# Kernel tuning notes

Hardware: AMD Instinct MI355X
Metric: run time of the kernel (lower is better)

Reference implementation:

```python
import jax, jax.numpy as jnp
import numpy as np

B, T, D, H, OUT = 4096, 48, 59, 256, 1


def _uni(k, shape, fan_in):
    s = 1.0 / np.sqrt(fan_in)
    return jax.random.uniform(k, shape, jnp.float32, -s, s)


def setup_inputs() -> dict:
    key = jax.random.key(0)
    ks = jax.random.split(key, 16)
    return {
        "x": jax.random.normal(ks[0], (B, T, D), jnp.float32),
        "mask": (jax.random.uniform(ks[1], (B, T, D)) < 0.7).astype(jnp.float32),
        "deltas": jax.random.uniform(ks[2], (B, T, D), jnp.float32) * 5.0,
        "last_obs": jax.random.normal(ks[3], (B, D), jnp.float32),
        "h": jax.random.normal(ks[4], (B, H), jnp.float32) * 0.1,
        "medians": jnp.zeros((D,), jnp.float32),  # medians_df=None -> zeros
        # Decay temp_decay_h (non-diag)
        "W_dh": _uni(ks[5], (H, D), D), "b_dh": jnp.zeros((H,), jnp.float32),
        # Decay temp_decay_x (diag, input==output)
        "W_dx": _uni(ks[6], (D, D), D), "b_dx": jnp.zeros((D,), jnp.float32),
        # hist: Linear(H, D)
        "hist_W": _uni(ks[7], (D, H), H), "hist_b": jnp.zeros((D,), jnp.float32),
        "feat_W": _uni(ks[8], (D, D), D), "feat_b": jnp.zeros((D,), jnp.float32),
        # weight_combine: Linear(2D, D)
        "wcomb_W": _uni(ks[9], (D, 2 * D), 2 * D), "wcomb_b": jnp.zeros((D,), jnp.float32),
        # Decay_obs linear (D, D)
        "wobs_W": _uni(ks[10], (D, D), D), "wobs_b": jnp.zeros((D,), jnp.float32),
        # GRUCell(2D, H)
        "W_ih": _uni(ks[11], (3 * H, 2 * D), 2 * D),
        "W_hh": _uni(ks[12], (3 * H, H), H),
        "b_ih": jnp.zeros((3 * H,), jnp.float32),
        "b_hh": jnp.zeros((3 * H,), jnp.float32),
        # classification: Linear(H, OUT)
        "cls_W": _uni(ks[13], (OUT, H), H), "cls_b": jnp.zeros((OUT,), jnp.float32),
    }


def reference(x, mask, deltas, last_obs, h, medians,
              W_dh, b_dh, W_dx, b_dx, hist_W, hist_b, feat_W, feat_b,
              wcomb_W, wcomb_b, wobs_W, wobs_b,
              W_ih, W_hh, b_ih, b_hh, cls_W, cls_b):
    Dn = x.shape[-1]
    Hn = h.shape[-1]
    eye = jnp.eye(Dn, dtype=x.dtype)

    # Decay_obs: sign-gated tanh weighting of (deltas - medians)
    dd = deltas - medians[None, None, :]
    wd = jnp.einsum('btd,ed->bte', dd, wobs_W) + wobs_b
    # relu(wd) + relu(-wd) == |wd|
    decay_factor = 0.5 * (1.0 - jnp.tanh(jnp.sign(dd) * jnp.abs(wd)))  # [B,T,D]

    dx_diag = jnp.diagonal(W_dx)          # diag decay: W * eye
    feat_Wm = feat_W * (1.0 - eye)

    def step(h, ins):
        x_t, m_t, d_t = ins               # each [B,D]
        gamma_h = jnp.exp(-jax.nn.relu(d_t @ W_dh.T + b_dh))   # [B,H]
        h = h * gamma_h
        x_h = h @ hist_W.T + hist_b                              # history estimate [B,D]
        x_r = m_t * x_t + (1.0 - m_t) * x_h                      # complemented input
        xu = x_r @ feat_Wm.T + feat_b
        gamma_x = jnp.exp(-jax.nn.relu(d_t * dx_diag + b_dx))    # diag decay [B,D]
        beta = jax.nn.sigmoid(
            jnp.concatenate([gamma_x, m_t], axis=-1) @ wcomb_W.T + wcomb_b)
        x_comb = beta * xu + (1.0 - beta) * x_h
        loss_t = jnp.sum(jnp.abs(x_t - x_comb) * m_t) / (jnp.sum(m_t) + 1e-5)
        x_imp_t = m_t * x_t + (1.0 - m_t) * x_comb
        # GRUCell with input concat([x_imp_t, m_t])
        gi = jnp.concatenate([x_imp_t, m_t], axis=-1) @ W_ih.T + b_ih
        gh = h @ W_hh.T + b_hh
        r = jax.nn.sigmoid(gi[:, :Hn] + gh[:, :Hn])
        z = jax.nn.sigmoid(gi[:, Hn:2 * Hn] + gh[:, Hn:2 * Hn])
        n = jnp.tanh(gi[:, 2 * Hn:] + r * gh[:, 2 * Hn:])
        h_new = (1.0 - z) * n + z * h
        return h_new, (x_imp_t, h_new, loss_t)

    xs = (x.transpose(1, 0, 2), mask.transpose(1, 0, 2), deltas.transpose(1, 0, 2))
    h_last, (x_imp, hs, losses) = jax.lax.scan(step, h, xs)
    x_imp = x_imp.transpose(1, 0, 2)          # [B,T,D]
    hidden_states = hs.transpose(1, 0, 2)     # [B,T,H]
    x_loss = jnp.sum(losses)
    y_out = h_last @ cls_W.T + cls_b          # dropout = identity at eval
    y_score = jax.nn.sigmoid(y_out)
    return x_imp, x_loss, hidden_states, y_out, y_score, decay_factor
```

## Files before the change

kernel.cpp:

```cpp
#include <hip/hip_runtime.h>
#include <math.h>

#define BATCH 4096
#define TT 48
#define DDIM 59
#define HHID 256
#define RR 16
#define NWG (BATCH/RR)
#define NTHR 1024

typedef _Float16 f16;
typedef _Float16 f16x8 __attribute__((ext_vector_type(8)));
typedef float    f32x4 __attribute__((ext_vector_type(4)));

static constexpr size_t N_XIMP   = (size_t)BATCH*TT*DDIM;
static constexpr size_t OFF_LOSS = N_XIMP;
static constexpr size_t OFF_HS   = OFF_LOSS + 1;
static constexpr size_t N_HS     = (size_t)BATCH*TT*HHID;
static constexpr size_t OFF_YOUT = OFF_HS + N_HS;
static constexpr size_t OFF_YSC  = OFF_YOUT + BATCH;
static constexpr size_t OFF_DEC  = OFF_YSC + BATCH;

static constexpr size_t WOFF_GRU  = 0;
static constexpr size_t WOFF_DH   = 294912;
static constexpr size_t WOFF_HIST = 311296;
static constexpr size_t WOFF_FEAT = 327680;
static constexpr size_t WOFF_WC   = 331776;

__device__ __forceinline__ float sigm(float v){ return 1.f/(1.f+expf(-v)); }

__global__ __launch_bounds__(256) void decay_kernel(
    const float* __restrict__ deltas, const float* __restrict__ medians,
    const float* __restrict__ wobs_W, const float* __restrict__ wobs_b,
    float* __restrict__ out_decay)
{
  __shared__ float sW[DDIM][60];
  __shared__ float sb[64], smed[64];
  __shared__ float sdd[16][60];
  const int tid = threadIdx.x;
  for (int idx = tid; idx < DDIM*DDIM; idx += 256){
    int e = idx/DDIM, d = idx - e*DDIM;
    sW[e][d] = wobs_W[idx];
  }
  if (tid < DDIM){ sb[tid] = wobs_b[tid]; smed[tid] = medians[tid]; }
  __syncthreads();
  const size_t row0 = (size_t)blockIdx.x * 16;
  for (int idx = tid; idx < 16*DDIM; idx += 256){
    int r = idx/DDIM, d = idx - r*DDIM;
    sdd[r][d] = __builtin_nontemporal_load(&deltas[(row0+r)*DDIM + d]) - smed[d];
  }
  __syncthreads();
  for (int idx = tid; idx < 16*DDIM; idx += 256){
    int r = idx/DDIM, e = idx - r*DDIM;
    float acc = sb[e];
    for (int d = 0; d < DDIM; d++) acc += sdd[r][d]*sW[e][d];
    float dd = sdd[r][e];
    float sg = (dd > 0.f) ? 1.f : ((dd < 0.f) ? -1.f : 0.f);
    out_decay[(row0+r)*DDIM + e] = 0.5f*(1.f - tanhf(sg*fabsf(acc)));
  }
}

__global__ __launch_bounds__(256) void conv_kernel(
    const float* __restrict__ W_dh, const float* __restrict__ hist_W,
    const float* __restrict__ feat_W, const float* __restrict__ wcomb_W,
    const float* __restrict__ W_ih, const float* __restrict__ W_hh,
    f16* __restrict__ ws)
{
  const int g  = blockIdx.x*4 + (threadIdx.x >> 6);
  const int l  = threadIdx.x & 63;
  const int nl = l & 15;
  const int kh = (l >> 4) * 8;
  f16x8 out;
  if (g < 576){
    int jb = g/36, s = g - jb*36;
    if (s < 24){
      int gate = s/12, kt = s - gate*12;
      int row  = gate*256 + jb*16 + nl;
      #pragma unroll
      for (int e = 0; e < 8; e++){
        int k = kt*32 + kh + e;
        float v = (k < 256) ? W_hh[(size_t)row*256 + k]
                : (k < 374) ? W_ih[(size_t)row*118 + (k-256)] : 0.f;
        out[e] = (f16)v;
      }
    } else if (s < 32){
      int kt = s - 24, row = 512 + jb*16 + nl;
      #pragma unroll
      for (int e = 0; e < 8; e++){
        int k = kt*32 + kh + e;
        out[e] = (f16)W_hh[(size_t)row*256 + k];
      }
    } else {
      int kt = s - 32, row = 512 + jb*16 + nl;
      #pragma unroll
      for (int e = 0; e < 8; e++){
        int k = kt*32 + kh + e;
        out[e] = (f16)((k < 118) ? W_ih[(size_t)row*118 + k] : 0.f);
      }
    }
    *(f16x8*)&ws[WOFF_GRU + (size_t)g*512 + l*8] = out;
  } else if (g < 608){
    int i = g - 576, nt = i >> 1, kt = i & 1;
    int row = nt*16 + nl;
    #pragma unroll
    for (int e = 0; e < 8; e++){
      int k = kt*32 + kh + e;
      out[e] = (f16)((k < 59) ? W_dh[(size_t)row*59 + k] : 0.f);
    }
    *(f16x8*)&ws[WOFF_DH + (size_t)i*512 + l*8] = out;
  } else if (g < 640){
    int i = g - 608, nt = i >> 3, kt = i & 7;
    int n = nt*16 + nl;
    #pragma unroll
    for (int e = 0; e < 8; e++){
      int k = kt*32 + kh + e;
      out[e] = (f16)((n < 59) ? hist_W[(size_t)n*256 + k] : 0.f);
    }
    *(f16x8*)&ws[WOFF_HIST + (size_t)i*512 + l*8] = out;
  } else if (g < 648){
    int i = g - 640, nt = i >> 1, kt = i & 1;
    int n = nt*16 + nl;
    #pragma unroll
    for (int e = 0; e < 8; e++){
      int k = kt*32 + kh + e;
      out[e] = (f16)((n < 59 && k < 59 && k != n) ? feat_W[(size_t)n*59 + k] : 0.f);
    }
    *(f16x8*)&ws[WOFF_FEAT + (size_t)i*512 + l*8] = out;
  } else {
    int i = g - 648, nt = i >> 2, kt = i & 3;
    int n = nt*16 + nl;
    #pragma unroll
    for (int e = 0; e < 8; e++){
      int k = kt*32 + kh + e;
      out[e] = (f16)((n < 59 && k < 118) ? wcomb_W[(size_t)n*118 + k] : 0.f);
    }
    *(f16x8*)&ws[WOFF_WC + (size_t)i*512 + l*8] = out;
  }
}

__global__ __launch_bounds__(NTHR) void seq_kernel(
    const float* __restrict__ x, const float* __restrict__ mask,
    const float* __restrict__ deltas, const float* __restrict__ h0,
    const float* __restrict__ b_dh, const float* __restrict__ W_dx,
    const float* __restrict__ b_dx, const float* __restrict__ hist_b,
    const float* __restrict__ feat_b, const float* __restrict__ wcomb_b,
    const float* __restrict__ b_ih, const float* __restrict__ b_hh,
    const f16* __restrict__ wb,
    float* __restrict__ out_ximp, float* __restrict__ out_hs,
    float* __restrict__ ws_num, float* __restrict__ ws_den)
{
  __shared__ f16 Acat[RR*392];
  __shared__ f16 AdAxr[RR*72];
  __shared__ f16 Agm [RR*136];
  __shared__ f16 ssx [RR*60];
  __shared__ f16 sxh [RR*60];
  __shared__ f16 sxu [RR*60];
  __shared__ f16 sbt [RR*60];
  __shared__ float sh [RR*260];
  __shared__ float sdiag[64], sbdx[64];
  __shared__ float sredN[16], sredD[16];

  const int tid = threadIdx.x;
  const int w   = tid >> 6;
  const int l   = tid & 63;
  const int nl  = l & 15;
  const int kh  = (l >> 4) * 8;
  const int mq  = (l >> 4) * 4;
  const int row0 = blockIdx.x * RR;

  const f16* Bgru  = wb + WOFF_GRU;
  const f16* Bdh   = wb + WOFF_DH;
  const f16* Bhist = wb + WOFF_HIST;
  const f16* Bfeat = wb + WOFF_FEAT;
  const f16* Bwc   = wb + WOFF_WC;
  const f16* Bb    = Bgru + (size_t)w*36*512;

  const bool hasS = (tid < RR*DDIM);
  const int r0s = tid/59, d0s = tid - r0s*59;

  const int nG = w*16 + nl;
  const float bdh_n = b_dh[nG];
  const float br_j  = b_ih[nG]     + b_hh[nG];
  const float bz_j  = b_ih[256+nG] + b_hh[256+nG];
  const float bni_j = b_ih[512+nG];
  const float bnh_j = b_hh[512+nG];
  const int nA = w*16 + nl;
  const int nB = (w-4)*16 + nl;
  const float hb_n = (w < 4 && nA < DDIM) ? hist_b[nA] : 0.f;
  const float fb_n = (w < 4 && nA < DDIM) ? feat_b[nA] : 0.f;
  const float cb_n = (w >= 4 && w < 8 && nB < DDIM) ? wcomb_b[nB] : 0.f;

  if (tid < DDIM){ sdiag[tid] = W_dx[(size_t)tid*DDIM + tid]; sbdx[tid] = b_dx[tid]; }
  for (int idx = tid; idx < RR*18; idx += NTHR){
    int r = idx/18, c = idx - (idx/18)*18;
    Acat[r*392 + 374 + c] = (f16)0.f;
    Agm [r*136 + 118 + c] = (f16)0.f;
  }
  for (int idx = tid; idx < RR*13; idx += NTHR){
    int r = idx/13, c = idx - (idx/13)*13;
    AdAxr[r*72 + 59 + c] = (f16)0.f;
  }
  for (int idx = tid; idx < RR*HHID; idx += NTHR){
    int r = idx >> 8, j = idx & 255;
    sh[r*260 + j] = h0[(size_t)(row0+r)*HHID + j];
  }

  float vx0 = 0.f, vm0 = 0.f, vd0 = 0.f;
  if (hasS){
    size_t g0 = ((size_t)(row0+r0s)*TT)*DDIM + d0s;
    vx0 = __builtin_nontemporal_load(&x[g0]);
    vm0 = __builtin_nontemporal_load(&mask[g0]);
    vd0 = __builtin_nontemporal_load(&deltas[g0]);
  }
  __syncthreads();

  for (int t = 0; t < TT; t++){
    if (hasS){
      ssx[r0s*60+d0s] = (f16)vx0;
      AdAxr[r0s*72+d0s] = (f16)vd0;
      Agm[r0s*136+59+d0s] = (f16)vm0;
      Acat[r0s*392+315+d0s] = (f16)vm0;
    }
    __syncthreads();

    if (t + 1 < TT && hasS){
      size_t g0 = ((size_t)(row0+r0s)*TT + (t+1))*DDIM + d0s;
      vx0 = __builtin_nontemporal_load(&x[g0]);
      vm0 = __builtin_nontemporal_load(&mask[g0]);
      vd0 = __builtin_nontemporal_load(&deltas[g0]);
    }

    {
      f32x4 acc = {0.f,0.f,0.f,0.f};
      #pragma unroll
      for (int kt = 0; kt < 2; kt++){
        f16x8 a = *(const f16x8*)&AdAxr[nl*72 + kt*32 + kh];
        f16x8 b = *(const f16x8*)&Bdh[(size_t)(w*2+kt)*512 + l*8];
        acc = __builtin_amdgcn_mfma_f32_16x16x32_f16(a, b, acc, 0, 0, 0);
      }
      #pragma unroll
      for (int q = 0; q < 4; q++){
        float gm = expf(-fmaxf(acc[q] + bdh_n, 0.f));
        float hv = sh[(mq+q)*260 + nG] * gm;
        sh[(mq+q)*260 + nG] = hv;
        Acat[(mq+q)*392 + nG] = (f16)hv;
      }
      if (hasS){
        float dv = (float)AdAxr[r0s*72 + d0s];
        float gx = expf(-fmaxf(dv*sdiag[d0s] + sbdx[d0s], 0.f));
        Agm[r0s*136 + d0s] = (f16)gx;
      }
    }
    __syncthreads();

    f32x4 gr = {0.f,0.f,0.f,0.f}, gz = {0.f,0.f,0.f,0.f}, gnh = {0.f,0.f,0.f,0.f};
    {
      #pragma unroll
      for (int kt = 0; kt < 8; kt++){
        f16x8 a  = *(const f16x8*)&Acat[nl*392 + kt*32 + kh];
        f16x8 br = *(const f16x8*)&Bb[(size_t)kt*512 + l*8];
        f16x8 bz = *(const f16x8*)&Bb[(size_t)(12+kt)*512 + l*8];
        f16x8 bn = *(const f16x8*)&Bb[(size_t)(24+kt)*512 + l*8];
        gr  = __builtin_amdgcn_mfma_f32_16x16x32_f16(a, br, gr, 0, 0, 0);
        gz  = __builtin_amdgcn_mfma_f32_16x16x32_f16(a, bz, gz, 0, 0, 0);
        gnh = __builtin_amdgcn_mfma_f32_16x16x32_f16(a, bn, gnh, 0, 0, 0);
      }
      if (w < 4){
        f32x4 acc = {0.f,0.f,0.f,0.f};
        #pragma unroll
        for (int kt = 0; kt < 8; kt++){
          f16x8 a = *(const f16x8*)&Acat[nl*392 + kt*32 + kh];
          f16x8 b = *(const f16x8*)&Bhist[(size_t)(w*8+kt)*512 + l*8];
          acc = __builtin_amdgcn_mfma_f32_16x16x32_f16(a, b, acc, 0, 0, 0);
        }
        if (nA < DDIM){
          #pragma unroll
          for (int q = 0; q < 4; q++) sxh[(mq+q)*60 + nA] = (f16)(acc[q] + hb_n);
        }
      } else if (w < 8){
        f32x4 acc = {0.f,0.f,0.f,0.f};
        #pragma unroll
        for (int kt = 0; kt < 4; kt++){
          f16x8 a = *(const f16x8*)&Agm[nl*136 + kt*32 + kh];
          f16x8 b = *(const f16x8*)&Bwc[(size_t)((w-4)*4+kt)*512 + l*8];
          acc = __builtin_amdgcn_mfma_f32_16x16x32_f16(a, b, acc, 0, 0, 0);
        }
        if (nB < DDIM){
          #pragma unroll
          for (int q = 0; q < 4; q++) sbt[(mq+q)*60 + nB] = (f16)sigm(acc[q] + cb_n);
        }
      }
    }
    __syncthreads();

    if (hasS){
      float m  = (float)Acat[r0s*392 + 315 + d0s];
      float xr = m*(float)ssx[r0s*60+d0s] + (1.f-m)*(float)sxh[r0s*60+d0s];
      AdAxr[r0s*72+d0s] = (f16)xr;
    }
    __syncthreads();

    if (w < 4){
      f32x4 acc = {0.f,0.f,0.f,0.f};
      #pragma unroll
      for (int kt = 0; kt < 2; kt++){
        f16x8 a = *(const f16x8*)&AdAxr[nl*72 + kt*32 + kh];
        f16x8 b = *(const f16x8*)&Bfeat[(size_t)(w*2+kt)*512 + l*8];
        acc = __builtin_amdgcn_mfma_f32_16x16x32_f16(a, b, acc, 0, 0, 0);
      }
      if (nA < DDIM){
        #pragma unroll
        for (int q = 0; q < 4; q++) sxu[(mq+q)*60 + nA] = (f16)(acc[q] + fb_n);
      }
    }
    __syncthreads();

    float lnum = 0.f, lden = 0.f;
    if (hasS){
      float xh = (float)sxh[r0s*60+d0s], xu = (float)sxu[r0s*60+d0s];
      float bt = (float)sbt[r0s*60+d0s];
      float xc = bt*xu + (1.f-bt)*xh;
      float m  = (float)Acat[r0s*392 + 315 + d0s];
      float xv = (float)ssx[r0s*60+d0s];
      lnum = fabsf(xv - xc)*m;
      lden = m;
      float xi = m*xv + (1.f-m)*xc;
      Acat[r0s*392 + 256 + d0s] = (f16)xi;
      out_ximp[((size_t)(row0+r0s)*TT + t)*DDIM + d0s] = xi;
    }
    #pragma unroll
    for (int off = 32; off >= 1; off >>= 1){
      lnum += __shfl_xor(lnum, off);
      lden += __shfl_xor(lden, off);
    }
    if (l == 0){ sredN[w] = lnum; sredD[w] = lden; }
    __syncthreads();
    if (tid == 0){
      float a = 0.f, b = 0.f;
      #pragma unroll
      for (int k = 0; k < 16; k++){ a += sredN[k]; b += sredD[k]; }
      atomicAdd(&ws_num[t], a); atomicAdd(&ws_den[t], b);
    }

    {
      f32x4 gni = {0.f,0.f,0.f,0.f};
      #pragma unroll
      for (int kt = 8; kt < 12; kt++){
        f16x8 a  = *(const f16x8*)&Acat[nl*392 + kt*32 + kh];
        f16x8 br = *(const f16x8*)&Bb[(size_t)kt*512 + l*8];
        f16x8 bz = *(const f16x8*)&Bb[(size_t)(12+kt)*512 + l*8];
        f16x8 bn = *(const f16x8*)&Bb[(size_t)(32+kt-8)*512 + l*8];
        gr  = __builtin_amdgcn_mfma_f32_16x16x32_f16(a, br, gr, 0, 0, 0);
        gz  = __builtin_amdgcn_mfma_f32_16x16x32_f16(a, bz, gz, 0, 0, 0);
        gni = __builtin_amdgcn_mfma_f32_16x16x32_f16(a, bn, gni, 0, 0, 0);
      }
      #pragma unroll
      for (int q = 0; q < 4; q++){
        float rg = sigm(gr[q] + br_j);
        float zg = sigm(gz[q] + bz_j);
        float ng = tanhf(gni[q] + bni_j + rg*(gnh[q] + bnh_j));
        float hold = sh[(mq+q)*260 + nG];
        float hn = (1.f-zg)*ng + zg*hold;
        sh[(mq+q)*260 + nG] = hn;
        __builtin_nontemporal_store(hn, &out_hs[((size_t)(row0+mq+q)*TT + t)*HHID + nG]);
      }
    }
    __syncthreads();
  }
}

__global__ __launch_bounds__(256) void final_kernel(
    const float* __restrict__ hs, const float* __restrict__ cls_W,
    const float* __restrict__ cls_b, const float* __restrict__ ws_num,
    const float* __restrict__ ws_den, float* __restrict__ out)
{
  int b = blockIdx.x*256 + threadIdx.x;
  if (b < BATCH){
    const float* hr = hs + ((size_t)b*TT + (TT-1))*HHID;
    float acc = cls_b[0];
    for (int j = 0; j < HHID; j++) acc += hr[j]*cls_W[j];
    out[OFF_YOUT + b] = acc;
    out[OFF_YSC  + b] = sigm(acc);
  }
  if (blockIdx.x == 0 && threadIdx.x == 0){
    float s = 0.f;
    for (int tt = 0; tt < TT; tt++) s += ws_num[tt]/(ws_den[tt] + 1e-5f);
    out[OFF_LOSS] = s;
  }
}

extern "C" void kernel_launch(void* const* d_in, const int* in_sizes, int n_in,
                              void* d_out, int out_size, void* d_ws, size_t ws_size,
                              hipStream_t stream)
{
  const float* x       = (const float*)d_in[0];
  const float* mask_   = (const float*)d_in[1];
  const float* deltas  = (const float*)d_in[2];
  const float* h0      = (const float*)d_in[4];
  const float* medians = (const float*)d_in[5];
  const float* W_dh    = (const float*)d_in[6];
  const float* b_dh    = (const float*)d_in[7];
  const float* W_dx    = (const float*)d_in[8];
  const float* b_dx    = (const float*)d_in[9];
  const float* hist_W  = (const float*)d_in[10];
  const float* hist_b  = (const float*)d_in[11];
  const float* feat_W  = (const float*)d_in[12];
  const float* feat_b  = (const float*)d_in[13];
  const float* wcomb_W = (const float*)d_in[14];
  const float* wcomb_b = (const float*)d_in[15];
  const float* wobs_W  = (const float*)d_in[16];
  const float* wobs_b  = (const float*)d_in[17];
  const float* W_ih    = (const float*)d_in[18];
  const float* W_hh    = (const float*)d_in[19];
  const float* b_ih    = (const float*)d_in[20];
  const float* b_hh    = (const float*)d_in[21];
  const float* cls_W   = (const float*)d_in[22];
  const float* cls_b   = (const float*)d_in[23];

  float* out    = (float*)d_out;
  float* ws_num = (float*)d_ws;
  float* ws_den = ws_num + TT;
  f16*   wbase  = (f16*)((char*)d_ws + 512);

  hipMemsetAsync(d_ws, 0, 512, stream);

  conv_kernel<<<166, 256, 0, stream>>>(W_dh, hist_W, feat_W, wcomb_W,
                                       W_ih, W_hh, wbase);

  decay_kernel<<<BATCH*TT/16, 256, 0, stream>>>(deltas, medians, wobs_W, wobs_b,
                                                out + OFF_DEC);

  seq_kernel<<<NWG, NTHR, 0, stream>>>(x, mask_, deltas, h0,
      b_dh, W_dx, b_dx, hist_b, feat_b, wcomb_b, b_ih, b_hh, wbase,
      out , out + OFF_HS, ws_num, ws_den);

  final_kernel<<<BATCH/256, 256, 0, stream>>>(out + OFF_HS, cls_W, cls_b,
                                              ws_num, ws_den, out);
}
```

Measured before the change: 1.524 ms.

## Halve seq_kernel block to 512 threads with two output tiles per wave

```diff
diff --git a/kernel.cpp b/kernel.cpp
--- a/kernel.cpp
+++ b/kernel.cpp
@@ -7,7 +7,7 @@
 #define HHID 256
 #define RR 16
 #define NWG (BATCH/RR)
-#define NTHR 1024
+#define NTHR 512
 
 typedef _Float16 f16;
 typedef _Float16 f16x8 __attribute__((ext_vector_type(8)));
@@ -138,7 +138,7 @@
   }
 }
 
-__global__ __launch_bounds__(NTHR) void seq_kernel(
+__global__ __launch_bounds__(NTHR, 2) void seq_kernel(
     const float* __restrict__ x, const float* __restrict__ mask,
     const float* __restrict__ deltas, const float* __restrict__ h0,
     const float* __restrict__ b_dh, const float* __restrict__ W_dx,
@@ -150,15 +150,14 @@
     float* __restrict__ ws_num, float* __restrict__ ws_den)
 {
   __shared__ f16 Acat[RR*392];
-  __shared__ f16 AdAxr[RR*72];
+  __shared__ f16 Ad  [RR*72];
   __shared__ f16 Agm [RR*136];
   __shared__ f16 ssx [RR*60];
   __shared__ f16 sxh [RR*60];
   __shared__ f16 sxu [RR*60];
   __shared__ f16 sbt [RR*60];
   __shared__ float sh [RR*260];
-  __shared__ float sdiag[64], sbdx[64];
-  __shared__ float sredN[16], sredD[16];
+  __shared__ float sredN[8], sredD[8];
 
   const int tid = threadIdx.x;
   const int w   = tid >> 6;
@@ -173,24 +172,38 @@
   const f16* Bhist = wb + WOFF_HIST;
   const f16* Bfeat = wb + WOFF_FEAT;
   const f16* Bwc   = wb + WOFF_WC;
-  const f16* Bb    = Bgru + (size_t)w*36*512;
-
-  const bool hasS = (tid < RR*DDIM);
-  const int r0s = tid/59, d0s = tid - r0s*59;
-
-  const int nG = w*16 + nl;
-  const float bdh_n = b_dh[nG];
-  const float br_j  = b_ih[nG]     + b_hh[nG];
-  const float bz_j  = b_ih[256+nG] + b_hh[256+nG];
-  const float bni_j = b_ih[512+nG];
-  const float bnh_j = b_hh[512+nG];
+
+  const int r0s = tid/59,        d0s = tid - r0s*59;
+  const int i1  = tid + NTHR;
+  const int r1s = i1/59,         d1s = i1 - r1s*59;
+  const bool has1 = (i1 < RR*DDIM);
+
+  const float dg0 = W_dx[(size_t)d0s*DDIM + d0s], bx0 = b_dx[d0s];
+  const float dg1 = has1 ? W_dx[(size_t)d1s*DDIM + d1s] : 0.f;
+  const float bx1 = has1 ? b_dx[d1s] : 0.f;
+
+  float bdh_i[2], br_j[2], bz_j[2], bni_j[2], bnh_j[2];
+  #pragma unroll
+  for (int ii = 0; ii < 2; ii++){
+    int n = (2*w+ii)*16 + nl;
+    bdh_i[ii] = b_dh[n];
+    br_j[ii]  = b_ih[n]     + b_hh[n];
+    bz_j[ii]  = b_ih[256+n] + b_hh[256+n];
+    bni_j[ii] = b_ih[512+n];
+    bnh_j[ii] = b_hh[512+n];
+  }
   const int nA = w*16 + nl;
   const int nB = (w-4)*16 + nl;
   const float hb_n = (w < 4 && nA < DDIM) ? hist_b[nA] : 0.f;
   const float fb_n = (w < 4 && nA < DDIM) ? feat_b[nA] : 0.f;
-  const float cb_n = (w >= 4 && w < 8 && nB < DDIM) ? wcomb_b[nB] : 0.f;
-
-  if (tid < DDIM){ sdiag[tid] = W_dx[(size_t)tid*DDIM + tid]; sbdx[tid] = b_dx[tid]; }
+  const float cb_n = (w >= 4 && nB < DDIM) ? wcomb_b[nB] : 0.f;
+
+  const int hrowA = tid >> 6;
+  const int hrowB = hrowA + 8;
+  const int hj0   = (tid & 63) * 4;
+  float* hsA = out_hs + (size_t)(row0+hrowA)*TT*HHID + hj0;
+  float* hsB = out_hs + (size_t)(row0+hrowB)*TT*HHID + hj0;
+
   for (int idx = tid; idx < RR*18; idx += NTHR){
     int r = idx/18, c = idx - (idx/18)*18;
     Acat[r*392 + 374 + c] = (f16)0.f;
@@ -198,93 +211,139 @@
   }
   for (int idx = tid; idx < RR*13; idx += NTHR){
     int r = idx/13, c = idx - (idx/13)*13;
-    AdAxr[r*72 + 59 + c] = (f16)0.f;
+    Ad[r*72 + 59 + c] = (f16)0.f;
   }
   for (int idx = tid; idx < RR*HHID; idx += NTHR){
     int r = idx >> 8, j = idx & 255;
     sh[r*260 + j] = h0[(size_t)(row0+r)*HHID + j];
   }
 
-  float vx0 = 0.f, vm0 = 0.f, vd0 = 0.f;
-  if (hasS){
+  float vx0, vm0, vd0, vx1 = 0.f, vm1 = 0.f, vd1 = 0.f;
+  {
     size_t g0 = ((size_t)(row0+r0s)*TT)*DDIM + d0s;
     vx0 = __builtin_nontemporal_load(&x[g0]);
     vm0 = __builtin_nontemporal_load(&mask[g0]);
     vd0 = __builtin_nontemporal_load(&deltas[g0]);
+    if (has1){
+      size_t g1 = ((size_t)(row0+r1s)*TT)*DDIM + d1s;
+      vx1 = __builtin_nontemporal_load(&x[g1]);
+      vm1 = __builtin_nontemporal_load(&mask[g1]);
+      vd1 = __builtin_nontemporal_load(&deltas[g1]);
+    }
   }
   __syncthreads();
 
   for (int t = 0; t < TT; t++){
-    if (hasS){
-      ssx[r0s*60+d0s] = (f16)vx0;
-      AdAxr[r0s*72+d0s] = (f16)vd0;
+    {
+      ssx[r0s*60+d0s]     = (f16)vx0;
+      Ad [r0s*72+d0s]     = (f16)vd0;
       Agm[r0s*136+59+d0s] = (f16)vm0;
       Acat[r0s*392+315+d0s] = (f16)vm0;
+      Agm[r0s*136+d0s]    = (f16)expf(-fmaxf(vd0*dg0 + bx0, 0.f));
+      if (has1){
+        ssx[r1s*60+d1s]     = (f16)vx1;
+        Ad [r1s*72+d1s]     = (f16)vd1;
+        Agm[r1s*136+59+d1s] = (f16)vm1;
+        Acat[r1s*392+315+d1s] = (f16)vm1;
+        Agm[r1s*136+d1s]    = (f16)expf(-fmaxf(vd1*dg1 + bx1, 0.f));
+      }
+      if (t > 0){
+        f32x4 va, vb;
+        #pragma unroll
+        for (int c = 0; c < 4; c++){ va[c] = sh[hrowA*260 + hj0 + c]; vb[c] = sh[hrowB*260 + hj0 + c]; }
+        __builtin_nontemporal_store(va, (f32x4*)(hsA + (size_t)(t-1)*HHID));
+        __builtin_nontemporal_store(vb, (f32x4*)(hsB + (size_t)(t-1)*HHID));
+      }
     }
     __syncthreads();
 
-    if (t + 1 < TT && hasS){
+    if (t + 1 < TT){
       size_t g0 = ((size_t)(row0+r0s)*TT + (t+1))*DDIM + d0s;
       vx0 = __builtin_nontemporal_load(&x[g0]);
       vm0 = __builtin_nontemporal_load(&mask[g0]);
       vd0 = __builtin_nontemporal_load(&deltas[g0]);
+      if (has1){
+        size_t g1 = ((size_t)(row0+r1s)*TT + (t+1))*DDIM + d1s;
+        vx1 = __builtin_nontemporal_load(&x[g1]);
+        vm1 = __builtin_nontemporal_load(&mask[g1]);
+        vd1 = __builtin_nontemporal_load(&deltas[g1]);
+      }
     }
 
     {
-      f32x4 acc = {0.f,0.f,0.f,0.f};
-      #pragma unroll
-      for (int kt = 0; kt < 2; kt++){
-        f16x8 a = *(const f16x8*)&AdAxr[nl*72 + kt*32 + kh];
-        f16x8 b = *(const f16x8*)&Bdh[(size_t)(w*2+kt)*512 + l*8];
-        acc = __builtin_amdgcn_mfma_f32_16x16x32_f16(a, b, acc, 0, 0, 0);
-      }
-      #pragma unroll
-      for (int q = 0; q < 4; q++){
-        float gm = expf(-fmaxf(acc[q] + bdh_n, 0.f));
-        float hv = sh[(mq+q)*260 + nG] * gm;
-        sh[(mq+q)*260 + nG] = hv;
-        Acat[(mq+q)*392 + nG] = (f16)hv;
-      }
-      if (hasS){
-        float dv = (float)AdAxr[r0s*72 + d0s];
-        float gx = expf(-fmaxf(dv*sdiag[d0s] + sbdx[d0s], 0.f));
-        Agm[r0s*136 + d0s] = (f16)gx;
+      f16x8 a0 = *(const f16x8*)&Ad[nl*72 + kh];
+      f16x8 a1 = *(const f16x8*)&Ad[nl*72 + 32 + kh];
+      #pragma unroll
+      for (int ii = 0; ii < 2; ii++){
+        int nt = 2*w + ii;
+        f16x8 b0 = *(const f16x8*)&Bdh[(size_t)(nt*2+0)*512 + l*8];
+        f16x8 b1 = *(const f16x8*)&Bdh[(size_t)(nt*2+1)*512 + l*8];
+        f32x4 acc = {0.f,0.f,0.f,0.f};
+        acc = __builtin_amdgcn_mfma_f32_16x16x32_f16(a0, b0, acc, 0, 0, 0);
+        acc = __builtin_amdgcn_mfma_f32_16x16x32_f16(a1, b1, acc, 0, 0, 0);
+        int n = nt*16 + nl;
+        #pragma unroll
+        for (int q = 0; q < 4; q++){
+          float gm = expf(-fmaxf(acc[q] + bdh_i[ii], 0.f));
+          float hv = sh[(mq+q)*260 + n] * gm;
+          sh[(mq+q)*260 + n] = hv;
+          Acat[(mq+q)*392 + n] = (f16)hv;
+        }
       }
     }
     __syncthreads();
 
-    f32x4 gr = {0.f,0.f,0.f,0.f}, gz = {0.f,0.f,0.f,0.f}, gnh = {0.f,0.f,0.f,0.f};
+    f32x4 gr[2], gz[2], gnh[2];
     {
-      #pragma unroll
-      for (int kt = 0; kt < 8; kt++){
-        f16x8 a  = *(const f16x8*)&Acat[nl*392 + kt*32 + kh];
-        f16x8 br = *(const f16x8*)&Bb[(size_t)kt*512 + l*8];
-        f16x8 bz = *(const f16x8*)&Bb[(size_t)(12+kt)*512 + l*8];
-        f16x8 bn = *(const f16x8*)&Bb[(size_t)(24+kt)*512 + l*8];
-        gr  = __builtin_amdgcn_mfma_f32_16x16x32_f16(a, br, gr, 0, 0, 0);
-        gz  = __builtin_amdgcn_mfma_f32_16x16x32_f16(a, bz, gz, 0, 0, 0);
-        gnh = __builtin_amdgcn_mfma_f32_16x16x32_f16(a, bn, gnh, 0, 0, 0);
-      }
+      f16x8 aH[8];
+      #pragma unroll
+      for (int kt = 0; kt < 8; kt++)
+        aH[kt] = *(const f16x8*)&Acat[nl*392 + kt*32 + kh];
+
+      #pragma unroll
+      for (int jj = 0; jj < 2; jj++){
+        const f16* Bb = Bgru + (size_t)(2*w+jj)*36*512;
+        f16x8 br[8], bz[8], bn[8];
+        #pragma unroll
+        for (int kt = 0; kt < 8; kt++){
+          br[kt] = *(const f16x8*)&Bb[(size_t)kt*512 + l*8];
+          bz[kt] = *(const f16x8*)&Bb[(size_t)(12+kt)*512 + l*8];
+          bn[kt] = *(const f16x8*)&Bb[(size_t)(24+kt)*512 + l*8];
+        }
+        f32x4 r_ = {0.f,0.f,0.f,0.f}, z_ = {0.f,0.f,0.f,0.f}, n_ = {0.f,0.f,0.f,0.f};
+        #pragma unroll
+        for (int kt = 0; kt < 8; kt++){
+          r_ = __builtin_amdgcn_mfma_f32_16x16x32_f16(aH[kt], br[kt], r_, 0, 0, 0);
+          z_ = __builtin_amdgcn_mfma_f32_16x16x32_f16(aH[kt], bz[kt], z_, 0, 0, 0);
+          n_ = __builtin_amdgcn_mfma_f32_16x16x32_f16(aH[kt], bn[kt], n_, 0, 0, 0);
+        }
+        gr[jj] = r_; gz[jj] = z_; gnh[jj] = n_;
+      }
+
       if (w < 4){
+        f16x8 bh[8];
+        #pragma unroll
+        for (int kt = 0; kt < 8; kt++)
+          bh[kt] = *(const f16x8*)&Bhist[(size_t)(w*8+kt)*512 + l*8];
         f32x4 acc = {0.f,0.f,0.f,0.f};
         #pragma unroll
-        for (int kt = 0; kt < 8; kt++){
-          f16x8 a = *(const f16x8*)&Acat[nl*392 + kt*32 + kh];
-          f16x8 b = *(const f16x8*)&Bhist[(size_t)(w*8+kt)*512 + l*8];
-          acc = __builtin_amdgcn_mfma_f32_16x16x32_f16(a, b, acc, 0, 0, 0);
-        }
+        for (int kt = 0; kt < 8; kt++)
+          acc = __builtin_amdgcn_mfma_f32_16x16x32_f16(aH[kt], bh[kt], acc, 0, 0, 0);
         if (nA < DDIM){
           #pragma unroll
           for (int q = 0; q < 4; q++) sxh[(mq+q)*60 + nA] = (f16)(acc[q] + hb_n);
         }
-      } else if (w < 8){
+      } else {
+        f16x8 aG[4], bw[4];
+        #pragma unroll
+        for (int kt = 0; kt < 4; kt++){
+          aG[kt] = *(const f16x8*)&Agm[nl*136 + kt*32 + kh];
+          bw[kt] = *(const f16x8*)&Bwc[(size_t)((w-4)*4+kt)*512 + l*8];
+        }
         f32x4 acc = {0.f,0.f,0.f,0.f};
         #pragma unroll
-        for (int kt = 0; kt < 4; kt++){
-          f16x8 a = *(const f16x8*)&Agm[nl*136 + kt*32 + kh];
-          f16x8 b = *(const f16x8*)&Bwc[(size_t)((w-4)*4+kt)*512 + l*8];
-          acc = __builtin_amdgcn_mfma_f32_16x16x32_f16(a, b, acc, 0, 0, 0);
-        }
+        for (int kt = 0; kt < 4; kt++)
+          acc = __builtin_amdgcn_mfma_f32_16x16x32_f16(aG[kt], bw[kt], acc, 0, 0, 0);
         if (nB < DDIM){
           #pragma unroll
           for (int q = 0; q < 4; q++) sbt[(mq+q)*60 + nB] = (f16)sigm(acc[q] + cb_n);
@@ -293,40 +352,59 @@
     }
     __syncthreads();
 
-    if (hasS){
-      float m  = (float)Acat[r0s*392 + 315 + d0s];
-      float xr = m*(float)ssx[r0s*60+d0s] + (1.f-m)*(float)sxh[r0s*60+d0s];
-      AdAxr[r0s*72+d0s] = (f16)xr;
+    if (w < 4){
+      f16x8 bf0 = *(const f16x8*)&Bfeat[(size_t)(w*2+0)*512 + l*8];
+      f16x8 bf1 = *(const f16x8*)&Bfeat[(size_t)(w*2+1)*512 + l*8];
+      f16x8 a0, a1;
+      #pragma unroll
+      for (int e = 0; e < 8; e++){
+        int c0 = kh + e;
+        int c1 = 32 + kh + e;
+        float xr0 = 0.f, xr1 = 0.f;
+        if (c0 < DDIM){
+          float m = (float)Agm[nl*136 + 59 + c0];
+          xr0 = m*(float)ssx[nl*60 + c0] + (1.f-m)*(float)sxh[nl*60 + c0];
+        }
+        if (c1 < DDIM){
+          float m = (float)Agm[nl*136 + 59 + c1];
+          xr1 = m*(float)ssx[nl*60 + c1] + (1.f-m)*(float)sxh[nl*60 + c1];
+        }
+        a0[e] = (f16)xr0; a1[e] = (f16)xr1;
+      }
+      f32x4 acc = {0.f,0.f,0.f,0.f};
+      acc = __builtin_amdgcn_mfma_f32_16x16x32_f16(a0, bf0, acc, 0, 0, 0);
+      acc = __builtin_amdgcn_mfma_f32_16x16x32_f16(a1, bf1, acc, 0, 0, 0);
+      if (nA < DDIM){
+        #pragma unroll
+        for (int q = 0; q < 4; q++) sxu[(mq+q)*60 + nA] = (f16)(acc[q] + fb_n);
+      }
     }
     __syncthreads();
 
-    if (w < 4){
-      f32x4 acc = {0.f,0.f,0.f,0.f};
-      #pragma unroll
-      for (int kt = 0; kt < 2; kt++){
-        f16x8 a = *(const f16x8*)&AdAxr[nl*72 + kt*32 + kh];
-        f16x8 b = *(const f16x8*)&Bfeat[(size_t)(w*2+kt)*512 + l*8];
-        acc = __builtin_amdgcn_mfma_f32_16x16x32_f16(a, b, acc, 0, 0, 0);
-      }
-      if (nA < DDIM){
-        #pragma unroll
-        for (int q = 0; q < 4; q++) sxu[(mq+q)*60 + nA] = (f16)(acc[q] + fb_n);
-      }
-    }
-    __syncthreads();
-
     float lnum = 0.f, lden = 0.f;
-    if (hasS){
+    {
       float xh = (float)sxh[r0s*60+d0s], xu = (float)sxu[r0s*60+d0s];
       float bt = (float)sbt[r0s*60+d0s];
       float xc = bt*xu + (1.f-bt)*xh;
-      float m  = (float)Acat[r0s*392 + 315 + d0s];
+      float m  = (float)Agm[r0s*136 + 59 + d0s];
       float xv = (float)ssx[r0s*60+d0s];
       lnum = fabsf(xv - xc)*m;
       lden = m;
       float xi = m*xv + (1.f-m)*xc;
       Acat[r0s*392 + 256 + d0s] = (f16)xi;
       out_ximp[((size_t)(row0+r0s)*TT + t)*DDIM + d0s] = xi;
+      if (has1){
+        xh = (float)sxh[r1s*60+d1s]; xu = (float)sxu[r1s*60+d1s];
+        bt = (float)sbt[r1s*60+d1s];
+        xc = bt*xu + (1.f-bt)*xh;
+        m  = (float)Agm[r1s*136 + 59 + d1s];
+        xv = (float)ssx[r1s*60+d1s];
+        lnum += fabsf(xv - xc)*m;
+        lden += m;
+        xi = m*xv + (1.f-m)*xc;
+        Acat[r1s*392 + 256 + d1s] = (f16)xi;
+        out_ximp[((size_t)(row0+r1s)*TT + t)*DDIM + d1s] = xi;
+      }
     }
     #pragma unroll
     for (int off = 32; off >= 1; off >>= 1){
@@ -338,34 +416,54 @@
     if (tid == 0){
       float a = 0.f, b = 0.f;
       #pragma unroll
-      for (int k = 0; k < 16; k++){ a += sredN[k]; b += sredD[k]; }
+      for (int k = 0; k < 8; k++){ a += sredN[k]; b += sredD[k]; }
       atomicAdd(&ws_num[t], a); atomicAdd(&ws_den[t], b);
     }
 
     {
-      f32x4 gni = {0.f,0.f,0.f,0.f};
-      #pragma unroll
-      for (int kt = 8; kt < 12; kt++){
-        f16x8 a  = *(const f16x8*)&Acat[nl*392 + kt*32 + kh];
-        f16x8 br = *(const f16x8*)&Bb[(size_t)kt*512 + l*8];
-        f16x8 bz = *(const f16x8*)&Bb[(size_t)(12+kt)*512 + l*8];
-        f16x8 bn = *(const f16x8*)&Bb[(size_t)(32+kt-8)*512 + l*8];
-        gr  = __builtin_amdgcn_mfma_f32_16x16x32_f16(a, br, gr, 0, 0, 0);
-        gz  = __builtin_amdgcn_mfma_f32_16x16x32_f16(a, bz, gz, 0, 0, 0);
-        gni = __builtin_amdgcn_mfma_f32_16x16x32_f16(a, bn, gni, 0, 0, 0);
-      }
-      #pragma unroll
-      for (int q = 0; q < 4; q++){
-        float rg = sigm(gr[q] + br_j);
-        float zg = sigm(gz[q] + bz_j);
-        float ng = tanhf(gni[q] + bni_j + rg*(gnh[q] + bnh_j));
-        float hold = sh[(mq+q)*260 + nG];
-        float hn = (1.f-zg)*ng + zg*hold;
-        sh[(mq+q)*260 + nG] = hn;
-        __builtin_nontemporal_store(hn, &out_hs[((size_t)(row0+mq+q)*TT + t)*HHID + nG]);
+      f16x8 aT[4];
+      #pragma unroll
+      for (int k = 0; k < 4; k++)
+        aT[k] = *(const f16x8*)&Acat[nl*392 + (8+k)*32 + kh];
+      #pragma unroll
+      for (int jj = 0; jj < 2; jj++){
+        const f16* Bb = Bgru + (size_t)(2*w+jj)*36*512;
+        f16x8 br[4], bz[4], bn[4];
+        #pragma unroll
+        for (int k = 0; k < 4; k++){
+          br[k] = *(const f16x8*)&Bb[(size_t)(8+k)*512 + l*8];
+          bz[k] = *(const f16x8*)&Bb[(size_t)(20+k)*512 + l*8];
+          bn[k] = *(const f16x8*)&Bb[(size_t)(32+k)*512 + l*8];
+        }
+        f32x4 r_ = gr[jj], z_ = gz[jj];
+        f32x4 gni = {0.f,0.f,0.f,0.f};
+        #pragma unroll
+        for (int k = 0; k < 4; k++){
+          r_  = __builtin_amdgcn_mfma_f32_16x16x32_f16(aT[k], br[k], r_, 0, 0, 0);
+          z_  = __builtin_amdgcn_mfma_f32_16x16x32_f16(aT[k], bz[k], z_, 0, 0, 0);
+          gni = __builtin_amdgcn_mfma_f32_16x16x32_f16(aT[k], bn[k], gni, 0, 0, 0);
+        }
+        int j = (2*w+jj)*16 + nl;
+        #pragma unroll
+        for (int q = 0; q < 4; q++){
+          float rg = sigm(r_[q] + br_j[jj]);
+          float zg = sigm(z_[q] + bz_j[jj]);
+          float ng = tanhf(gni[q] + bni_j[jj] + rg*(gnh[jj][q] + bnh_j[jj]));
+          float hold = sh[(mq+q)*260 + j];
+          float hn = (1.f-zg)*ng + zg*hold;
+          sh[(mq+q)*260 + j] = hn;
+        }
       }
     }
     __syncthreads();
+  }
+
+  {
+    f32x4 va, vb;
+    #pragma unroll
+    for (int c = 0; c < 4; c++){ va[c] = sh[hrowA*260 + hj0 + c]; vb[c] = sh[hrowB*260 + hj0 + c]; }
+    __builtin_nontemporal_store(va, (f32x4*)(hsA + (size_t)(TT-1)*HHID));
+    __builtin_nontemporal_store(vb, (f32x4*)(hsB + (size_t)(TT-1)*HHID));
   }
 }
 
@@ -422,7 +520,7 @@
   float* ws_den = ws_num + TT;
   f16*   wbase  = (f16*)((char*)d_ws + 512);
 
-  hipMemsetAsync(d_ws, 0, 512, stream);
+  (void)hipMemsetAsync(d_ws, 0, 512, stream);
 
   conv_kernel<<<166, 256, 0, stream>>>(W_dh, hist_W, feat_W, wcomb_W,
                                        W_ih, W_hh, wbase);
```

New measurement: 1.626 ms. +6.7%, slower.
